# Kernel tuning notes

Hardware: AMD Instinct MI355X
Metric: run time of the kernel (lower is better)

The kernel has to match this reference:

```python
import jax, jax.numpy as jnp
import numpy as np

ALPHA = 0.5
GAMMA = 0.01
TOP_K = 5
B, T, C = 2048, 8192, 1  # C must be 1 for amp_loss's grouped conv1d to be valid


def _ashift_loss(inp, tgt):
    _, t_len, _ = inp.shape
    sm = jax.nn.softmax(inp - tgt, axis=1)                      # [B,T,C]
    return jnp.mean(jnp.sum(jnp.abs(1.0 / t_len - sm), axis=1, keepdims=True))


def _phase_loss(inp, tgt, top_k=TOP_K):
    inp_f = jnp.fft.rfft(inp, axis=1)                           # [B,Tf,C] complex
    tgt_f = jnp.fft.rfft(tgt, axis=1)
    b, tf_len, c = tgt_f.shape
    amp = jnp.abs(tgt_f).at[:, 0, :].set(0.0)                   # zero DC bin
    # top-k magnitudes along freq axis (per batch, per channel)
    _, idx = jax.lax.top_k(jnp.transpose(amp, (0, 2, 1)), top_k)  # [B,C,k]
    top = jnp.transpose(idx, (0, 2, 1))                         # [B,k,C]
    # boolean mask: True everywhere except top-k freq bins (per column)
    freqs = jnp.arange(tf_len)
    mask = ~jnp.any(freqs[None, :, None, None] == top[:, None, :, :], axis=2)  # [B,Tf,C]
    # replicate torch row-major boolean-mask flatten + view(B, Tf-k, C):
    flat = mask.reshape(b, tf_len * c)
    order = jnp.argsort(~flat, axis=1, stable=True)             # kept (True) positions first, in row-major order
    keep = order[:, : (tf_len - top_k) * c]                     # flat (t*C + c') positions
    non_top = (keep // c).reshape(b, tf_len - top_k, c)         # stored value is the freq index t
    dom = jnp.take_along_axis(tgt_f, top, axis=1) - jnp.take_along_axis(inp_f, top, axis=1)
    domain_loss = jnp.mean(jnp.sqrt(jnp.sum(jnp.abs(dom) ** 2, axis=1)))
    gath = jnp.take_along_axis(inp_f, non_top, axis=1)          # [B,Tf-k,C]
    nondomain_loss = jnp.mean(jnp.sqrt(jnp.sum(jnp.abs(gath) ** 2, axis=1, keepdims=True)))
    return domain_loss + nondomain_loss


def _amp_loss(inp, tgt):
    # Valid only for C==1: conv1d([B,1,T], weight=[B,1,T], groups=1) -> [B,B,1]
    # out[b,o] = sum_t tgt[b,t] * flip(kernel)[o,t]
    t2 = tgt[:, :, 0]                                           # [B,T]
    i2 = inp[:, :, 0]
    flip_diff = t2[:, ::-1] - i2[:, ::-1]                       # flip(target) - flip(input)
    diff = jnp.einsum('bt,ot->bo', t2, flip_diff)               # self_corr - cross_corr, [B,B]
    # torch.norm(p=2) over the singleton dim == abs
    return jnp.mean(jnp.abs(diff))


def setup_inputs() -> dict:
    key = jax.random.key(0)
    k1, k2 = jax.random.split(key)
    inp = jax.random.normal(k1, (B, T, C), dtype=jnp.float32)
    tgt = jax.random.normal(k2, (B, T, C), dtype=jnp.float32)
    return {"input": inp, "target": tgt}


def reference(input, target):
    return (ALPHA * _ashift_loss(input, target)
            + (1.0 - ALPHA) * _phase_loss(input, target)
            + GAMMA * _amp_loss(input, target))
```

## Files before the change

### kernel.cpp

```cpp
#include <hip/hip_runtime.h>
#include <hip/hip_bf16.h>
#include <math.h>

#define B_N 2048
#define T_N 8192
#define NFFT 4096
#define TF_LEN 4097
#define TOPK 5

#define ZIDX(n) ((n) + ((n) >> 4))
#define ZPAD (NFFT + (NFFT >> 4))

typedef float f32x4 __attribute__((ext_vector_type(4)));
typedef __bf16 bf16x8 __attribute__((ext_vector_type(8)));
typedef unsigned short ushort_t;

__device__ __forceinline__ void gload_lds16(const ushort_t* g, ushort_t* l) {
    __builtin_amdgcn_global_load_lds(
        (const __attribute__((address_space(1))) void*)g,
        (__attribute__((address_space(3))) void*)l,
        16, 0, 0);
}

__device__ __forceinline__ float wave_reduce_sum(float v) {
    for (int o = 32; o >= 1; o >>= 1) v += __shfl_xor(v, o, 64);
    return v;
}
__device__ __forceinline__ float wave_reduce_max(float v) {
    for (int o = 32; o >= 1; o >>= 1) v = fmaxf(v, __shfl_xor(v, o, 64));
    return v;
}

__device__ __forceinline__ ushort_t f2bf(float x) {
    __hip_bfloat16 h = __float2bfloat16(x);
    return *reinterpret_cast<ushort_t*>(&h);
}

__device__ __forceinline__ float2 cis_rev(float rev) {
    return make_float2(__builtin_amdgcn_cosf(rev), __builtin_amdgcn_sinf(rev));
}
__device__ __forceinline__ float2 cmulf(float2 a, float2 b) {
    return make_float2(a.x * b.x - a.y * b.y, a.x * b.y + a.y * b.x);
}

__global__ void init_kernel(float* acc) {
    if (threadIdx.x < 4) acc[threadIdx.x] = 0.0f;
}

__device__ __forceinline__ void dft4(float2 x0, float2 x1, float2 x2, float2 x3,
                                     float2* y0, float2* y1, float2* y2, float2* y3) {
    float2 t0 = make_float2(x0.x + x2.x, x0.y + x2.y);
    float2 t1 = make_float2(x0.x - x2.x, x0.y - x2.y);
    float2 t2 = make_float2(x1.x + x3.x, x1.y + x3.y);
    float2 t3 = make_float2(x1.x - x3.x, x1.y - x3.y);
    *y0 = make_float2(t0.x + t2.x, t0.y + t2.y);
    *y2 = make_float2(t0.x - t2.x, t0.y - t2.y);
    *y1 = make_float2(t1.x + t3.y, t1.y - t3.x);
    *y3 = make_float2(t1.x - t3.y, t1.y + t3.x);
}

__device__ __forceinline__ void dft16(float2 X[16]) {
    float2 G[16];
    dft4(X[0], X[4], X[8],  X[12], &G[0],  &G[1],  &G[2],  &G[3]);
    dft4(X[1], X[5], X[9],  X[13], &G[4],  &G[5],  &G[6],  &G[7]);
    dft4(X[2], X[6], X[10], X[14], &G[8],  &G[9],  &G[10], &G[11]);
    dft4(X[3], X[7], X[11], X[15], &G[12], &G[13], &G[14], &G[15]);
    const float C1 = 0.9238795325112867f, S1 = 0.3826834323650898f;
    const float R2 = 0.7071067811865476f;
    G[5]  = cmulf(G[5],  make_float2(C1, -S1));
    G[6]  = cmulf(G[6],  make_float2(R2, -R2));
    G[7]  = cmulf(G[7],  make_float2(S1, -C1));
    G[9]  = cmulf(G[9],  make_float2(R2, -R2));
    { float2 g = G[10]; G[10] = make_float2(g.y, -g.x); }
    G[11] = cmulf(G[11], make_float2(-R2, -R2));
    G[13] = cmulf(G[13], make_float2(S1, -C1));
    G[14] = cmulf(G[14], make_float2(-R2, -R2));
    G[15] = cmulf(G[15], make_float2(-C1, S1));
    dft4(G[0], G[4], G[8],  G[12], &X[0], &X[4], &X[8],  &X[12]);
    dft4(G[1], G[5], G[9],  G[13], &X[1], &X[5], &X[9],  &X[13]);
    dft4(G[2], G[6], G[10], G[14], &X[2], &X[6], &X[10], &X[14]);
    dft4(G[3], G[7], G[11], G[15], &X[3], &X[7], &X[11], &X[15]);
}

__device__ __forceinline__ void rfft_bin(const float2* Zs, int k, float* orr, float* oi) {
    int kk = k & (NFFT - 1);
    int nk = (NFFT - k) & (NFFT - 1);
    float2 zk = Zs[ZIDX(kk)], znk = Zs[ZIDX(nk)];
    float xer = 0.5f * (zk.x + znk.x);
    float xei = 0.5f * (zk.y - znk.y);
    float xo_r = 0.5f * (zk.y + znk.y);
    float xo_i = -0.5f * (zk.x - znk.x);
    float2 w = cis_rev((float)k * (-1.0f / (float)T_N));
    *orr = xer + w.x * xo_r - w.y * xo_i;
    *oi = xei + w.x * xo_i + w.y * xo_r;
}

__global__ __launch_bounds__(256) void fused_row_kernel(const float* __restrict__ inp,
                                                        const float* __restrict__ tgt,
                                                        ushort_t* __restrict__ Abf,
                                                        ushort_t* __restrict__ Bbf,
                                                        float* acc) {
    __shared__ float2 Zs[ZPAD];
    __shared__ __align__(16) float amp[TF_LEN];
    __shared__ float red[4];
    __shared__ float wv[4];
    __shared__ int wi[4];
    __shared__ int topIdx[TOPK];
    __shared__ float2 tgtF[TOPK];
    __shared__ float rscratch[64];

    int b = blockIdx.x;
    int tid = threadIdx.x;
    int lane = tid & 63, wid = tid >> 6;
    const float* tp = tgt + (size_t)b * T_N;
    const float* ip = inp + (size_t)b * T_N;
    ushort_t* Ab = Abf + (size_t)b * T_N;
    ushort_t* Bb = Bbf + (size_t)b * T_N;

    float4 trv[8];
#pragma unroll
    for (int i = 0; i < 8; i++) {
        int q = tid + 256 * i;
        trv[i] = *reinterpret_cast<const float4*>(&tp[4 * q]);
        ushort4 ua;
        ua.x = f2bf(trv[i].x); ua.y = f2bf(trv[i].y);
        ua.z = f2bf(trv[i].z); ua.w = f2bf(trv[i].w);
        *reinterpret_cast<ushort4*>(&Ab[4 * q]) = ua;
        int m0 = 2 * q, m1 = 2 * q + 1;
        int p0 = ((m0 & 15) << 8) | (m0 & 0x0F0) | (m0 >> 8);
        int p1 = ((m1 & 15) << 8) | (m1 & 0x0F0) | (m1 >> 8);
        Zs[ZIDX(p0)] = make_float2(trv[i].x, trv[i].y);
        Zs[ZIDX(p1)] = make_float2(trv[i].z, trv[i].w);
    }

    float4 irv[8], dv[8];
#pragma unroll
    for (int i = 0; i < 8; i++) {
        int q = tid + 256 * i;
        irv[i] = *reinterpret_cast<const float4*>(&ip[4 * q]);
        dv[i] = make_float4(irv[i].x - trv[i].x, irv[i].y - trv[i].y,
                            irv[i].z - trv[i].z, irv[i].w - trv[i].w);
    }

    float* ampf = amp;
#pragma unroll
    for (int i = 0; i < 4; i++)
        *reinterpret_cast<float4*>(&ampf[4 * (tid + 256 * i)]) = dv[i];
    __syncthreads();
#pragma unroll
    for (int i2 = 0; i2 < 4; i2++) {
        int qr = 1024 + tid + 256 * i2;
        float4 v = *reinterpret_cast<const float4*>(&ampf[4 * (1023 - tid - 256 * i2)]);
        ushort4 ub;
        ub.x = f2bf(-v.w); ub.y = f2bf(-v.z); ub.z = f2bf(-v.y); ub.w = f2bf(-v.x);
        *reinterpret_cast<ushort4*>(&Bb[4 * qr]) = ub;
    }
    __syncthreads();
#pragma unroll
    for (int i = 4; i < 8; i++)
        *reinterpret_cast<float4*>(&ampf[4 * (tid + 256 * (i - 4))]) = dv[i];
    __syncthreads();
#pragma unroll
    for (int i2 = 0; i2 < 4; i2++) {
        int qr = tid + 256 * i2;
        float4 v = *reinterpret_cast<const float4*>(&ampf[4 * (1023 - tid - 256 * i2)]);
        ushort4 ub;
        ub.x = f2bf(-v.w); ub.y = f2bf(-v.z); ub.z = f2bf(-v.y); ub.w = f2bf(-v.x);
        *reinterpret_cast<ushort4*>(&Bb[4 * qr]) = ub;
    }
    __syncthreads();

    {
        float lmax = -1e30f;
#pragma unroll
        for (int i = 0; i < 8; i++)
            lmax = fmaxf(lmax, fmaxf(fmaxf(dv[i].x, dv[i].y), fmaxf(dv[i].z, dv[i].w)));
        lmax = wave_reduce_max(lmax);
        if (lane == 0) red[wid] = lmax;
        __syncthreads();
        float mx = fmaxf(fmaxf(red[0], red[1]), fmaxf(red[2], red[3]));
        __syncthreads();
        float lsum = 0.0f;
#pragma unroll
        for (int i = 0; i < 8; i++) {
            dv[i].x = __expf(dv[i].x - mx);
            dv[i].y = __expf(dv[i].y - mx);
            dv[i].z = __expf(dv[i].z - mx);
            dv[i].w = __expf(dv[i].w - mx);
            lsum += (dv[i].x + dv[i].y) + (dv[i].z + dv[i].w);
        }
        lsum = wave_reduce_sum(lsum);
        if (lane == 0) red[wid] = lsum;
        __syncthreads();
        float Z = (red[0] + red[1]) + (red[2] + red[3]);
        __syncthreads();
        float inv = 1.0f / Z;
        const float u = 1.0f / (float)T_N;
        float labs = 0.0f;
#pragma unroll
        for (int i = 0; i < 8; i++) {
            labs += fabsf(u - dv[i].x * inv) + fabsf(u - dv[i].y * inv) +
                    fabsf(u - dv[i].z * inv) + fabsf(u - dv[i].w * inv);
        }
        labs = wave_reduce_sum(labs);
        if (lane == 0) red[wid] = labs;
        __syncthreads();
        if (tid == 0)
            atomicAdd(acc + 0, (red[0] + red[1]) + (red[2] + red[3]));
    }
    __syncthreads();

    {
        float2 X[16];
        int base = tid * 16;
#pragma unroll
        for (int r = 0; r < 16; r++) X[r] = Zs[ZIDX(base + r)];
        dft16(X);
#pragma unroll
        for (int r = 0; r < 16; r++) Zs[ZIDX(base + r)] = X[r];
    }
    __syncthreads();
    {
        float2 X[16];
        int j = tid & 15;
        int base = (tid >> 4) * 256 + j;
#pragma unroll
        for (int r = 0; r < 16; r++) X[r] = Zs[ZIDX(base + 16 * r)];
        float2 w1 = cis_rev(-(float)j * (1.0f / 256.0f));
        float2 w = w1;
#pragma unroll
        for (int r = 1; r < 16; r++) { X[r] = cmulf(X[r], w); w = cmulf(w, w1); }
        dft16(X);
#pragma unroll
        for (int r = 0; r < 16; r++) Zs[ZIDX(base + 16 * r)] = X[r];
    }
    __syncthreads();
    {
        float2 X[16];
#pragma unroll
        for (int r = 0; r < 16; r++) X[r] = Zs[ZIDX(tid + 256 * r)];
        float2 w1 = cis_rev(-(float)tid * (1.0f / 4096.0f));
        float2 w = w1;
#pragma unroll
        for (int r = 1; r < 16; r++) { X[r] = cmulf(X[r], w); w = cmulf(w, w1); }
        dft16(X);
#pragma unroll
        for (int r = 0; r < 16; r++) Zs[ZIDX(tid + 256 * r)] = X[r];
    }
    __syncthreads();

    {
        float2 rot = cis_rev(-(float)tid * (1.0f / (float)T_N));
        const float2 drot = make_float2(0.9807852804032304f, -0.19509032201612825f);
#pragma unroll
        for (int i = 0; i < 16; i++) {
            int k = tid + 256 * i;
            if (k == 0) {
                amp[0] = -1.0f;
            } else {
                int nk = (NFFT - k) & (NFFT - 1);
                float2 zk = Zs[ZIDX(k & (NFFT - 1))], znk = Zs[ZIDX(nk)];
                float xer = 0.5f * (zk.x + znk.x);
                float xei = 0.5f * (zk.y - znk.y);
                float xo_r = 0.5f * (zk.y + znk.y);
                float xo_i = -0.5f * (zk.x - znk.x);
                float xr = xer + rot.x * xo_r - rot.y * xo_i;
                float xi = xei + rot.x * xo_i + rot.y * xo_r;
                amp[k] = xr * xr + xi * xi;
            }
            rot = cmulf(rot, drot);
        }
        if (tid == 0) {
            float2 z0 = Zs[ZIDX(0)];
            float v = z0.x - z0.y;
            amp[4096] = v * v;
        }
    }
    __syncthreads();

    for (int r = 0; r < TOPK; r++) {
        float bv = -3.0f;
        int bi = TF_LEN;
        for (int k = tid; k < TF_LEN; k += 256) {
            float a = amp[k];
            if (a > bv) { bv = a; bi = k; }
        }
        for (int o = 1; o < 64; o <<= 1) {
            float ov = __shfl_xor(bv, o, 64);
            int oi = __shfl_xor(bi, o, 64);
            if (ov > bv || (ov == bv && oi < bi)) { bv = ov; bi = oi; }
        }
        if (lane == 0) { wv[wid] = bv; wi[wid] = bi; }
        __syncthreads();
        if (tid == 0) {
            float fv = wv[0];
            int fi = wi[0];
            for (int w = 1; w < 4; w++)
                if (wv[w] > fv || (wv[w] == fv && wi[w] < fi)) { fv = wv[w]; fi = wi[w]; }
            topIdx[r] = fi;
            amp[fi] = -2.0f;
        }
        __syncthreads();
    }

    if (tid < TOPK) {
        float xr, xi;
        rfft_bin(Zs, topIdx[tid], &xr, &xi);
        tgtF[tid] = make_float2(xr, xi);
    }
    __syncthreads();

    int fq[TOPK];
#pragma unroll
    for (int q = 0; q < TOPK; q++) fq[q] = topIdx[q];

    float2 cur[TOPK], wc[TOPK], wf[TOPK];
    float re[TOPK], im[TOPK];
#pragma unroll
    for (int q = 0; q < TOPK; q++) {
        int f = fq[q];
        cur[q] = cis_rev(-(float)((f * 4 * tid) & (T_N - 1)) * (1.0f / (float)T_N));
        wc[q] = cis_rev(-(float)f * (1.0f / (float)T_N));
        wf[q] = cis_rev(-(float)((f * 1021) & (T_N - 1)) * (1.0f / (float)T_N));
        re[q] = 0.0f; im[q] = 0.0f;
    }
    float E = 0.0f, sev = 0.0f, sod = 0.0f;
#pragma unroll
    for (int i = 0; i < 8; i++) {
        float vv0 = irv[i].x, vv1 = irv[i].y, vv2 = irv[i].z, vv3 = irv[i].w;
        E = fmaf(vv0, vv0, E); sev += vv0;
#pragma unroll
        for (int q = 0; q < TOPK; q++) {
            re[q] = fmaf(vv0, cur[q].x, re[q]); im[q] = fmaf(vv0, cur[q].y, im[q]);
            cur[q] = cmulf(cur[q], wc[q]);
        }
        E = fmaf(vv1, vv1, E); sod += vv1;
#pragma unroll
        for (int q = 0; q < TOPK; q++) {
            re[q] = fmaf(vv1, cur[q].x, re[q]); im[q] = fmaf(vv1, cur[q].y, im[q]);
            cur[q] = cmulf(cur[q], wc[q]);
        }
        E = fmaf(vv2, vv2, E); sev += vv2;
#pragma unroll
        for (int q = 0; q < TOPK; q++) {
            re[q] = fmaf(vv2, cur[q].x, re[q]); im[q] = fmaf(vv2, cur[q].y, im[q]);
            cur[q] = cmulf(cur[q], wc[q]);
        }
        E = fmaf(vv3, vv3, E); sod += vv3;
#pragma unroll
        for (int q = 0; q < TOPK; q++) {
            re[q] = fmaf(vv3, cur[q].x, re[q]); im[q] = fmaf(vv3, cur[q].y, im[q]);
            cur[q] = cmulf(cur[q], wf[q]);
        }
    }

    float vals[13] = {re[0], im[0], re[1], im[1], re[2], im[2], re[3], im[3],
                      re[4], im[4], E, sev + sod, sev - sod};
#pragma unroll
    for (int i = 0; i < 13; i++) {
        float v = wave_reduce_sum(vals[i]);
        if (lane == 0) rscratch[wid * 13 + i] = v;
    }
    __syncthreads();
    if (tid == 0) {
        float tot[13];
        for (int i = 0; i < 13; i++)
            tot[i] = rscratch[i] + rscratch[13 + i] + rscratch[26 + i] + rscratch[39 + i];
        float dsum = 0, isum = 0;
        for (int q = 0; q < TOPK; q++) {
            float rr = tot[2 * q], ii = tot[2 * q + 1];
            float dr = tgtF[q].x - rr, di = tgtF[q].y - ii;
            dsum += dr * dr + di * di;
            isum += rr * rr + ii * ii;
        }
        float Ee = tot[10], X0v = tot[11], Xhv = tot[12];
        float S_all = 0.5f * ((float)T_N * Ee + X0v * X0v + Xhv * Xhv);
        float val = sqrtf(dsum) + sqrtf(fmaxf(S_all - isum, 0.0f));
        atomicAdd(acc + 1, val);
    }
}

__global__ __launch_bounds__(512) void gemm_kernel(const ushort_t* __restrict__ A,
                                                   const ushort_t* __restrict__ Bm,
                                                   float* acc) {
    __shared__ __align__(16) ushort_t sA[2][128 * 32];
    __shared__ __align__(16) ushort_t sB[2][128 * 32];
    __shared__ float scratch[8];
    const int K = T_N;
    const int NSTEP = K / 32;
    int tid = threadIdx.x;

    int bid = blockIdx.x;
    int swz = ((bid & 7) << 5) | (bid >> 3);
    int bx = swz >> 4, by = swz & 15;
    int row0 = bx * 128, col0 = by * 128;

    int w = tid >> 6, lane = tid & 63;
    int wm = w >> 2, wn = w & 3;
    int lr = lane & 15, kq = lane >> 4;

    f32x4 accf[4][2];
#pragma unroll
    for (int mi = 0; mi < 4; mi++)
#pragma unroll
        for (int ni = 0; ni < 2; ni++) accf[mi][ni] = (f32x4){0.f, 0.f, 0.f, 0.f};

    int r_st = tid >> 2, c_st = (tid & 3) * 8;
    const ushort_t* gA = A + (size_t)(row0 + r_st) * K + c_st;
    const ushort_t* gB = Bm + (size_t)(col0 + r_st) * K + c_st;
    ushort_t* lA0 = &sA[0][tid * 8];
    ushort_t* lA1 = &sA[1][tid * 8];
    ushort_t* lB0 = &sB[0][tid * 8];
    ushort_t* lB1 = &sB[1][tid * 8];

    int aoff = (wm * 64 + lr) * 32 + kq * 8;
    int boff = (wn * 32 + lr) * 32 + kq * 8;

    gload_lds16(gA, lA0);
    gload_lds16(gB, lB0);
    asm volatile("s_waitcnt vmcnt(0)" ::: "memory");
    __builtin_amdgcn_s_barrier();

    for (int t = 0; t < NSTEP; ++t) {
        int cur = t & 1;
        if (t + 1 < NSTEP) {
            int k0 = (t + 1) * 32;
            gload_lds16(gA + k0, cur ? lA0 : lA1);
            gload_lds16(gB + k0, cur ? lB0 : lB1);
        }

        const ushort_t* ap = (cur ? sA[1] : sA[0]) + aoff;
        const ushort_t* bp = (cur ? sB[1] : sB[0]) + boff;
        bf16x8 af[4], bfr[2];
#pragma unroll
        for (int mi = 0; mi < 4; mi++)
            af[mi] = *reinterpret_cast<const bf16x8*>(ap + mi * 16 * 32);
#pragma unroll
        for (int ni = 0; ni < 2; ni++)
            bfr[ni] = *reinterpret_cast<const bf16x8*>(bp + ni * 16 * 32);
#pragma unroll
        for (int mi = 0; mi < 4; mi++)
#pragma unroll
            for (int ni = 0; ni < 2; ni++)
                accf[mi][ni] = __builtin_amdgcn_mfma_f32_16x16x32_bf16(
                    af[mi], bfr[ni], accf[mi][ni], 0, 0, 0);

        asm volatile("s_waitcnt vmcnt(0)" ::: "memory");
        __builtin_amdgcn_s_barrier();
    }

    float s = 0.0f;
#pragma unroll
    for (int mi = 0; mi < 4; mi++)
#pragma unroll
        for (int ni = 0; ni < 2; ni++)
#pragma unroll
            for (int r = 0; r < 4; r++) s += fabsf(accf[mi][ni][r]);
    s = wave_reduce_sum(s);
    if (lane == 0) scratch[w] = s;
    __syncthreads();
    if (tid == 0) {
        float tot = 0.0f;
        for (int i = 0; i < 8; i++) tot += scratch[i];
        atomicAdd(acc, tot);
    }
}

__global__ void combine_kernel(const float* acc, float* out) {
    if (threadIdx.x == 0) {
        float ash = acc[0] / (float)B_N;
        float ph = acc[1] / (float)B_N;
        float am = acc[2] / ((float)B_N * (float)B_N);
        out[0] = 0.5f * ash + 0.5f * ph + 0.01f * am;
    }
}

extern "C" void kernel_launch(void* const* d_in, const int* in_sizes, int n_in,
                              void* d_out, int out_size, void* d_ws, size_t ws_size,
                              hipStream_t stream) {
    const float* inp = (const float*)d_in[0];
    const float* tgt = (const float*)d_in[1];
    float* acc = (float*)d_ws;
    ushort_t* Abf = (ushort_t*)((char*)d_ws + 256);
    ushort_t* Bbf = Abf + (size_t)B_N * T_N;
    float* out = (float*)d_out;

    hipLaunchKernelGGL(init_kernel, dim3(1), dim3(64), 0, stream, acc);
    hipLaunchKernelGGL(fused_row_kernel, dim3(B_N), dim3(256), 0, stream,
                       inp, tgt, Abf, Bbf, acc);
    hipLaunchKernelGGL(gemm_kernel, dim3(256), dim3(512), 0, stream, Abf, Bbf, acc + 2);
    hipLaunchKernelGGL(combine_kernel, dim3(1), dim3(1), 0, stream, acc, out);
}
```

Measured before the change: 199.1 us.

## Deepen GEMM K-tile to 64 with triple-buffered swizzled LDS pipeline

Restructures the bf16 MFMA GEMM main loop so each step covers a K-tile of 64 instead of 32, with three LDS buffers and prefetch issued two stages ahead. Partial vmcnt waits replace the full drain, and the barrier count is halved. An XOR swizzle on LDS columns is meant to avoid bank conflicts on fragment reads, and s_setprio is raised around the MFMA block. The cost is triple the LDS footprint, 96KB, which may limit occupancy, plus more registers for the doubled fragment sets.

```diff
diff --git a/kernel.cpp b/kernel.cpp
--- a/kernel.cpp
+++ b/kernel.cpp
@@ -383,11 +383,11 @@
 __global__ __launch_bounds__(512) void gemm_kernel(const ushort_t* __restrict__ A,
                                                    const ushort_t* __restrict__ Bm,
                                                    float* acc) {
-    __shared__ __align__(16) ushort_t sA[2][128 * 32];
-    __shared__ __align__(16) ushort_t sB[2][128 * 32];
+    __shared__ __align__(16) ushort_t sA[3][128 * 64];
+    __shared__ __align__(16) ushort_t sB[3][128 * 64];
     __shared__ float scratch[8];
     const int K = T_N;
-    const int NSTEP = K / 32;
+    const int NSTEP = K / 64;
     int tid = threadIdx.x;
 
     int bid = blockIdx.x;
@@ -405,49 +405,87 @@
 #pragma unroll
         for (int ni = 0; ni < 2; ni++) accf[mi][ni] = (f32x4){0.f, 0.f, 0.f, 0.f};
 
-    int r_st = tid >> 2, c_st = (tid & 3) * 8;
-    const ushort_t* gA = A + (size_t)(row0 + r_st) * K + c_st;
-    const ushort_t* gB = Bm + (size_t)(col0 + r_st) * K + c_st;
-    ushort_t* lA0 = &sA[0][tid * 8];
-    ushort_t* lA1 = &sA[1][tid * 8];
-    ushort_t* lB0 = &sB[0][tid * 8];
-    ushort_t* lB1 = &sB[1][tid * 8];
-
-    int aoff = (wm * 64 + lr) * 32 + kq * 8;
-    int boff = (wn * 32 + lr) * 32 + kq * 8;
-
-    gload_lds16(gA, lA0);
-    gload_lds16(gB, lB0);
-    asm volatile("s_waitcnt vmcnt(0)" ::: "memory");
-    __builtin_amdgcn_s_barrier();
+    int strow = tid >> 3;
+    int scb = (tid & 7) ^ (strow & 7);
+    const ushort_t* gA0 = A + (size_t)(row0 + strow) * K + scb * 8;
+    const ushort_t* gA1 = A + (size_t)(row0 + 64 + strow) * K + scb * 8;
+    const ushort_t* gB0 = Bm + (size_t)(col0 + strow) * K + scb * 8;
+    const ushort_t* gB1 = Bm + (size_t)(col0 + 64 + strow) * K + scb * 8;
+    int ldst0 = tid * 8;
+    int ldst1 = 4096 + tid * 8;
+
+    int aoffs[2][4], boffs[2][2];
+#pragma unroll
+    for (int kk = 0; kk < 2; kk++) {
+#pragma unroll
+        for (int mi = 0; mi < 4; mi++) {
+            int row = wm * 64 + mi * 16 + lr;
+            aoffs[kk][mi] = row * 64 + (((kk * 4 + kq) ^ (lr & 7)) << 3);
+        }
+#pragma unroll
+        for (int ni = 0; ni < 2; ni++) {
+            int row = wn * 32 + ni * 16 + lr;
+            boffs[kk][ni] = row * 64 + (((kk * 4 + kq) ^ (lr & 7)) << 3);
+        }
+    }
+
+#define STAGE(bi, k0)                                  \
+    do {                                               \
+        gload_lds16(gA0 + (k0), &sA[bi][ldst0]);       \
+        gload_lds16(gA1 + (k0), &sA[bi][ldst1]);       \
+        gload_lds16(gB0 + (k0), &sB[bi][ldst0]);       \
+        gload_lds16(gB1 + (k0), &sB[bi][ldst1]);       \
+    } while (0)
+
+    STAGE(0, 0);
+    STAGE(1, 64);
 
     for (int t = 0; t < NSTEP; ++t) {
-        int cur = t & 1;
-        if (t + 1 < NSTEP) {
-            int k0 = (t + 1) * 32;
-            gload_lds16(gA + k0, cur ? lA0 : lA1);
-            gload_lds16(gB + k0, cur ? lB0 : lB1);
-        }
-
-        const ushort_t* ap = (cur ? sA[1] : sA[0]) + aoff;
-        const ushort_t* bp = (cur ? sB[1] : sB[0]) + boff;
-        bf16x8 af[4], bfr[2];
+        if (t + 1 < NSTEP)
+            asm volatile("s_waitcnt vmcnt(4)" ::: "memory");
+        else
+            asm volatile("s_waitcnt vmcnt(0)" ::: "memory");
+        __builtin_amdgcn_s_barrier();
+        __builtin_amdgcn_sched_barrier(0);
+
+        if (t + 2 < NSTEP) {
+            int bi = (t + 2) % 3;
+            int k0 = (t + 2) * 64;
+            STAGE(bi, k0);
+        }
+
+        const ushort_t* As = sA[t % 3];
+        const ushort_t* Bs = sB[t % 3];
+        bf16x8 af0[4], bf0[2], af1[4], bf1[2];
 #pragma unroll
         for (int mi = 0; mi < 4; mi++)
-            af[mi] = *reinterpret_cast<const bf16x8*>(ap + mi * 16 * 32);
+            af0[mi] = *reinterpret_cast<const bf16x8*>(As + aoffs[0][mi]);
 #pragma unroll
         for (int ni = 0; ni < 2; ni++)
-            bfr[ni] = *reinterpret_cast<const bf16x8*>(bp + ni * 16 * 32);
+            bf0[ni] = *reinterpret_cast<const bf16x8*>(Bs + boffs[0][ni]);
+#pragma unroll
+        for (int mi = 0; mi < 4; mi++)
+            af1[mi] = *reinterpret_cast<const bf16x8*>(As + aoffs[1][mi]);
+#pragma unroll
+        for (int ni = 0; ni < 2; ni++)
+            bf1[ni] = *reinterpret_cast<const bf16x8*>(Bs + boffs[1][ni]);
+
+        __builtin_amdgcn_s_setprio(1);
 #pragma unroll
         for (int mi = 0; mi < 4; mi++)
 #pragma unroll
             for (int ni = 0; ni < 2; ni++)
                 accf[mi][ni] = __builtin_amdgcn_mfma_f32_16x16x32_bf16(
-                    af[mi], bfr[ni], accf[mi][ni], 0, 0, 0);
-
-        asm volatile("s_waitcnt vmcnt(0)" ::: "memory");
-        __builtin_amdgcn_s_barrier();
-    }
+                    af0[mi], bf0[ni], accf[mi][ni], 0, 0, 0);
+#pragma unroll
+        for (int mi = 0; mi < 4; mi++)
+#pragma unroll
+            for (int ni = 0; ni < 2; ni++)
+                accf[mi][ni] = __builtin_amdgcn_mfma_f32_16x16x32_bf16(
+                    af1[mi], bf1[ni], accf[mi][ni], 0, 0, 0);
+        __builtin_amdgcn_s_setprio(0);
+    }
+#undef STAGE
 
     float s = 0.0f;
 #pragma unroll
```

Result: no change. 202.4 us (+1.7%).
